# Performance work log

Hardware: AMD Instinct MI355X
Metric: run time of the kernel (lower is better)

The kernel has to match this reference:

```python
import jax, jax.numpy as jnp
import numpy as np

B, S, H, OUT = 4096, 200, 512, 64


def setup_inputs() -> dict:
    key = jax.random.key(0)
    ks = jax.random.split(key, 16)
    sc = 0.05
    return {
        "last_input": jax.random.normal(ks[0], (B, OUT), jnp.float32),
        "hidden": jax.random.normal(ks[1], (1, B, H), jnp.float32),
        "encoder_outputs": jax.random.normal(ks[2], (S, B, H), jnp.float32),
        "attn_W": jax.random.normal(ks[3], (S, H + OUT), jnp.float32) * sc,
        "attn_b": jax.random.normal(ks[4], (S,), jnp.float32) * sc,
        "comb_W": jax.random.normal(ks[5], (H, H + OUT), jnp.float32) * sc,
        "comb_b": jax.random.normal(ks[6], (H,), jnp.float32) * sc,
        "w_ih": jax.random.normal(ks[7], (3 * H, H), jnp.float32) * sc,
        "w_hh": jax.random.normal(ks[8], (3 * H, H), jnp.float32) * sc,
        "b_ih": jax.random.normal(ks[9], (3 * H,), jnp.float32) * sc,
        "b_hh": jax.random.normal(ks[10], (3 * H,), jnp.float32) * sc,
        "out_W": jax.random.normal(ks[11], (OUT, H), jnp.float32) * sc,
        "out_b": jax.random.normal(ks[12], (OUT,), jnp.float32) * sc,
    }


def reference(last_input, hidden, encoder_outputs, attn_W, attn_b, comb_W,
              comb_b, w_ih, w_hh, b_ih, b_hh, out_W, out_b):
    h0 = hidden[0]  # [B,H]
    # Bahdanau-style attention scores over the encoder sequence
    cat1 = jnp.concatenate([last_input, h0], axis=1)          # [B, OUT+H]
    attn_weights = jax.nn.softmax(cat1 @ attn_W.T + attn_b, axis=1)  # [B,S]
    enc = jnp.transpose(encoder_outputs, (1, 0, 2))            # [B,S,H]
    attn_applied = jnp.einsum('bs,bsh->bh', attn_weights, enc)  # [B,H]
    # combine + relu
    cat2 = jnp.concatenate([last_input, attn_applied], axis=1)  # [B, OUT+H]
    x = jax.nn.relu(cat2 @ comb_W.T + comb_b)                   # [B,H]
    # single-step GRU (PyTorch gate order: r, z, n)
    gi = x @ w_ih.T + b_ih                                      # [B,3H]
    gh = h0 @ w_hh.T + b_hh                                     # [B,3H]
    i_r, i_z, i_n = jnp.split(gi, 3, axis=1)
    h_r, h_z, h_n = jnp.split(gh, 3, axis=1)
    r = jax.nn.sigmoid(i_r + h_r)
    z = jax.nn.sigmoid(i_z + h_z)
    n = jnp.tanh(i_n + r * h_n)
    h_new = (1.0 - z) * n + z * h0                              # [B,H]
    out = h_new @ out_W.T + out_b                               # [B,OUT]
    return out, h_new[None], attn_weights
```

## Files before the change

### kernel.cpp

```cpp
#include <hip/hip_runtime.h>
#include <cstddef>

constexpr int Bn = 4096;
constexpr int Sn = 200;
constexpr int Hn = 512;
constexpr int On = 64;
constexpr int K1 = 576;

constexpr size_t HNEW_OFF = (size_t)Bn * On;
constexpr size_t AW_OFF   = (size_t)Bn * On + (size_t)Bn * Hn;

constexpr size_t CAT1B_OFF = 0;
constexpr size_t CAT2B_OFF = CAT1B_OFF + (size_t)Bn * K1 * 2;
constexpr size_t XB_OFF    = CAT2B_OFF + (size_t)Bn * K1 * 2;
constexpr size_t WIHB_OFF  = XB_OFF    + (size_t)Bn * Hn * 2;
constexpr size_t WHHB_OFF  = WIHB_OFF  + (size_t)3 * Hn * Hn * 2;
constexpr size_t CWB_OFF   = WHHB_OFF  + (size_t)3 * Hn * Hn * 2;
constexpr size_t OWB_OFF   = CWB_OFF   + (size_t)Hn * K1 * 2;
constexpr size_t AWB_OFF   = OWB_OFF   + (size_t)On * Hn * 2;
constexpr size_t LOG_OFF   = AWB_OFF   + (size_t)256 * K1 * 2;
constexpr size_t HNB_OFF   = LOG_OFF   + (size_t)Bn * Sn * 4;

typedef __attribute__((ext_vector_type(8))) short bf16x8;
typedef __attribute__((ext_vector_type(4))) float f32x4;

__device__ __forceinline__ float sigmoidf_(float v) { return 1.f / (1.f + __expf(-v)); }
__device__ __forceinline__ unsigned short f2bf(float f) {
    unsigned u = __float_as_uint(f);
    return (unsigned short)((u + 0x7FFFu + ((u >> 16) & 1u)) >> 16);
}
__device__ __forceinline__ ushort4 pack4(float4 v) {
    ushort4 o = { f2bf(v.x), f2bf(v.y), f2bf(v.z), f2bf(v.w) };
    return o;
}

__global__ __launch_bounds__(256) void cvt_all_kernel(
    const float* __restrict__ hidden, const float* __restrict__ wih,
    const float* __restrict__ whh, const float* __restrict__ combW,
    const float* __restrict__ outW, const float* __restrict__ attnW,
    const float* __restrict__ li,
    unsigned short* __restrict__ cat1b, unsigned short* __restrict__ cat2b,
    unsigned short* __restrict__ wihb, unsigned short* __restrict__ whhb,
    unsigned short* __restrict__ combWb, unsigned short* __restrict__ outWb,
    unsigned short* __restrict__ awWb)
{
    const int blk = blockIdx.x;
    const int t = threadIdx.x;
    if (blk < 2048) {
        size_t off = (size_t)blk * 1024 + (size_t)t * 4;
        int b = (int)(off >> 9), col = (int)(off & 511);
        float4 v = *(const float4*)(hidden + off);
        *(ushort4*)(cat1b + (size_t)b * K1 + On + col) = pack4(v);
    } else if (blk < 3584) {
        size_t off = (size_t)(blk - 2048) * 1024 + (size_t)t * 4;
        const float* s = (blk < 2816) ? wih : whh;
        unsigned short* d = (blk < 2816) ? wihb : whhb;
        if (blk >= 2816) off -= (size_t)768 * 1024;
        float4 v = *(const float4*)(s + off);
        *(ushort4*)(d + off) = pack4(v);
    } else if (blk < 3872) {
        size_t off = (size_t)(blk - 3584) * 1024 + (size_t)t * 4;
        float4 v = *(const float4*)(combW + off);
        *(ushort4*)(combWb + off) = pack4(v);
    } else if (blk < 3904) {
        size_t off = (size_t)(blk - 3872) * 1024 + (size_t)t * 4;
        float4 v = *(const float4*)(outW + off);
        *(ushort4*)(outWb + off) = pack4(v);
    } else if (blk < 4017) {
        size_t off = (size_t)(blk - 3904) * 1024 + (size_t)t * 4;
        if (off < (size_t)Sn * K1) {
            float4 v = *(const float4*)(attnW + off);
            *(ushort4*)(awWb + off) = pack4(v);
        }
    } else if (blk < 4049) {
        size_t off = (size_t)Sn * K1 + (size_t)(blk - 4017) * 1024 + (size_t)t * 4;
        if (off < (size_t)256 * K1) {
            ushort4 z = {0, 0, 0, 0};
            *(ushort4*)(awWb + off) = z;
        }
    } else {
        size_t off = (size_t)(blk - 4049) * 1024 + (size_t)t * 4;
        int b = (int)(off >> 6), col = (int)(off & 63);
        float4 v = *(const float4*)(li + off);
        ushort4 o = pack4(v);
        *(ushort4*)(cat1b + (size_t)b * K1 + col) = o;
        *(ushort4*)(cat2b + (size_t)b * K1 + col) = o;
    }
}

template<int MF, int NF, bool RELU, bool OUT_BF16>
__device__ __forceinline__ void gemm_bt_body(
    const unsigned short* __restrict__ A, int lda,
    const unsigned short* __restrict__ B,
    const float* __restrict__ bias, float* __restrict__ Cf,
    unsigned short* __restrict__ Cb, int K, int ldc,
    int m0, int n0, int nmax)
{
    constexpr int BM = 32 * MF;
    constexpr int BN = 32 * NF;
    __shared__ unsigned short As[BM * 64];
    __shared__ unsigned short Bs[BN * 64];

    const int tid = threadIdx.x;
    const int wave = tid >> 6;
    const int lane = tid & 63;
    const int wm = wave >> 1, wn = wave & 1;
    const int l15 = lane & 15, lg = lane >> 4;

    f32x4 acc[MF][NF];
#pragma unroll
    for (int i = 0; i < MF; ++i)
#pragma unroll
        for (int j = 0; j < NF; ++j) acc[i][j] = (f32x4){0.f, 0.f, 0.f, 0.f};

    for (int kc = 0; kc < K; kc += 64) {
        __syncthreads();
#pragma unroll
        for (int i = 0; i < BM * 8 / 256; ++i) {
            int idx = tid + i * 256;
            int row = idx >> 3, ck = idx & 7;
            uint4 v = *(const uint4*)(A + (size_t)(m0 + row) * lda + kc + ck * 8);
            int byte = row * 128 + ((ck * 16) ^ ((row & 7) << 4));
            *(uint4*)((char*)As + byte) = v;
        }
#pragma unroll
        for (int i = 0; i < BN * 8 / 256; ++i) {
            int idx = tid + i * 256;
            int row = idx >> 3, ck = idx & 7;
            uint4 v = *(const uint4*)(B + (size_t)(n0 + row) * K + kc + ck * 8);
            int byte = row * 128 + ((ck * 16) ^ ((row & 7) << 4));
            *(uint4*)((char*)Bs + byte) = v;
        }
        __syncthreads();
#pragma unroll
        for (int s = 0; s < 2; ++s) {
            bf16x8 af[MF], bfr[NF];
#pragma unroll
            for (int i = 0; i < MF; ++i) {
                int row = wm * (MF * 16) + i * 16 + l15;
                int byte = row * 128 + ((s * 64 + lg * 16) ^ ((row & 7) << 4));
                af[i] = *(const bf16x8*)((const char*)As + byte);
            }
#pragma unroll
            for (int j = 0; j < NF; ++j) {
                int row = wn * (NF * 16) + j * 16 + l15;
                int byte = row * 128 + ((s * 64 + lg * 16) ^ ((row & 7) << 4));
                bfr[j] = *(const bf16x8*)((const char*)Bs + byte);
            }
#pragma unroll
            for (int i = 0; i < MF; ++i)
#pragma unroll
                for (int j = 0; j < NF; ++j)
                    acc[i][j] = __builtin_amdgcn_mfma_f32_16x16x32_bf16(
                        af[i], bfr[j], acc[i][j], 0, 0, 0);
        }
    }

#pragma unroll
    for (int i = 0; i < MF; ++i) {
        int m = m0 + wm * (MF * 16) + i * 16 + lg * 4;
#pragma unroll
        for (int j = 0; j < NF; ++j) {
            int n = n0 + wn * (NF * 16) + j * 16 + l15;
            if (n < nmax) {
                float bv = bias[n];
#pragma unroll
                for (int r = 0; r < 4; ++r) {
                    float v = acc[i][j][r] + bv;
                    if (RELU) v = fmaxf(v, 0.f);
                    if (OUT_BF16) Cb[(size_t)(m + r) * ldc + n] = f2bf(v);
                    else          Cf[(size_t)(m + r) * ldc + n] = v;
                }
            }
        }
    }
}

__global__ __launch_bounds__(256, 2) void scores_gemm_kernel(
    const unsigned short* __restrict__ cat1b, const unsigned short* __restrict__ awWb,
    const float* __restrict__ attn_b, float* __restrict__ logits)
{
    gemm_bt_body<2, 2, false, false>(cat1b, K1, awWb, attn_b, logits, nullptr,
                                     K1, Sn, blockIdx.x * 64, blockIdx.y * 64, Sn);
}

__global__ __launch_bounds__(256, 2) void comb_gemm_kernel(
    const unsigned short* __restrict__ cat2b, const unsigned short* __restrict__ combWb,
    const float* __restrict__ comb_b, unsigned short* __restrict__ xb)
{
    gemm_bt_body<4, 4, true, true>(cat2b, K1, combWb, comb_b, nullptr, xb,
                                   K1, Hn, blockIdx.x * 128, blockIdx.y * 128, Hn);
}

__global__ __launch_bounds__(256, 2) void out_gemm_kernel(
    const unsigned short* __restrict__ hnewb, const unsigned short* __restrict__ outWb,
    const float* __restrict__ out_b, float* __restrict__ dout)
{
    gemm_bt_body<4, 2, false, false>(hnewb, Hn, outWb, out_b, dout, nullptr,
                                     Hn, On, blockIdx.x * 128, 0, On);
}

__global__ __launch_bounds__(256) void softmax_kernel(
    const float* __restrict__ logits, float* __restrict__ dout)
{
    const int row = blockIdx.x * 4 + (threadIdx.x >> 6);
    const int lane = threadIdx.x & 63;
    const float* lp = logits + (size_t)row * Sn;
    float v[4], e[4];
    float m = -3.0e38f;
#pragma unroll
    for (int k = 0; k < 4; ++k) {
        int s = lane + 64 * k;
        v[k] = (s < Sn) ? lp[s] : -3.0e38f;
        m = fmaxf(m, v[k]);
    }
#pragma unroll
    for (int o = 32; o > 0; o >>= 1) m = fmaxf(m, __shfl_xor(m, o, 64));
    float sum = 0.f;
#pragma unroll
    for (int k = 0; k < 4; ++k) {
        int s = lane + 64 * k;
        e[k] = (s < Sn) ? __expf(v[k] - m) : 0.f;
        sum += e[k];
    }
#pragma unroll
    for (int o = 32; o > 0; o >>= 1) sum += __shfl_xor(sum, o, 64);
    float inv = 1.f / sum;
#pragma unroll
    for (int k = 0; k < 4; ++k) {
        int s = lane + 64 * k;
        if (s < Sn) dout[AW_OFF + (size_t)row * Sn + s] = e[k] * inv;
    }
}

__global__ __launch_bounds__(256) void attn_apply_kernel(
    const float* __restrict__ enc, const float* __restrict__ aw,
    unsigned short* __restrict__ cat2b)
{
    __shared__ float wl[8 * Sn];
    const int tid = threadIdx.x;
    const int b0 = blockIdx.x * 8;

    for (int idx = tid; idx < 8 * Sn; idx += 256)
        wl[idx] = aw[(size_t)b0 * Sn + idx];
    __syncthreads();

    const int q = tid >> 7;
    const int hc = tid & 127;
    const f32x4* base = (const f32x4*)enc + ((size_t)(b0 + q * 4)) * 128 + hc;

    f32x4 a0 = {0,0,0,0}, a1 = {0,0,0,0}, a2 = {0,0,0,0}, a3 = {0,0,0,0};

#pragma unroll 2
    for (int s = 0; s < Sn; ++s) {
        const f32x4* p = base + (size_t)s * (Bn * 128);
        f32x4 v0 = __builtin_nontemporal_load(p);
        f32x4 v1 = __builtin_nontemporal_load(p + 128);
        f32x4 v2 = __builtin_nontemporal_load(p + 256);
        f32x4 v3 = __builtin_nontemporal_load(p + 384);
        float w0 = wl[(q * 4 + 0) * Sn + s];
        float w1 = wl[(q * 4 + 1) * Sn + s];
        float w2 = wl[(q * 4 + 2) * Sn + s];
        float w3 = wl[(q * 4 + 3) * Sn + s];
        a0 += v0 * w0; a1 += v1 * w1; a2 += v2 * w2; a3 += v3 * w3;
    }

    const int h = hc * 4;
    f32x4 accs[4] = {a0, a1, a2, a3};
#pragma unroll
    for (int r = 0; r < 4; ++r) {
        ushort4 o = { f2bf(accs[r][0]), f2bf(accs[r][1]), f2bf(accs[r][2]), f2bf(accs[r][3]) };
        *(ushort4*)(cat2b + (size_t)(b0 + q * 4 + r) * K1 + On + h) = o;
    }
}

__device__ __forceinline__ void gru_gemm_phase(
    const unsigned short* __restrict__ A, int lda,
    const unsigned short* __restrict__ W,
    int m0, int n0, int tid, int wm, int wn, int l15, int lg,
    unsigned short* As, unsigned short* Bs,
    f32x4 aR[2][2], f32x4 aZ[2][2], f32x4 aN[2][2])
{
    for (int kc = 0; kc < Hn; kc += 64) {
        __syncthreads();
#pragma unroll
        for (int i = 0; i < 2; ++i) {
            int idx = tid + i * 256;
            int row = idx >> 3, ck = idx & 7;
            uint4 v = *(const uint4*)(A + (size_t)(m0 + row) * lda + kc + ck * 8);
            int byte = row * 128 + ((ck * 16) ^ ((row & 7) << 4));
            *(uint4*)((char*)As + byte) = v;
        }
#pragma unroll
        for (int g = 0; g < 3; ++g)
#pragma unroll
            for (int i = 0; i < 2; ++i) {
                int idx = tid + i * 256;
                int row = idx >> 3, ck = idx & 7;
                uint4 v = *(const uint4*)(W + (size_t)(g * Hn + n0 + row) * Hn + kc + ck * 8);
                int byte = row * 128 + ((ck * 16) ^ ((row & 7) << 4));
                *(uint4*)((char*)Bs + g * 8192 + byte) = v;
            }
        __syncthreads();
#pragma unroll
        for (int s = 0; s < 2; ++s) {
            bf16x8 af[2], bf0[2], bf1[2], bf2[2];
#pragma unroll
            for (int i = 0; i < 2; ++i) {
                int row = wm * 32 + i * 16 + l15;
                int byte = row * 128 + ((s * 64 + lg * 16) ^ ((row & 7) << 4));
                af[i] = *(const bf16x8*)((const char*)As + byte);
            }
#pragma unroll
            for (int j = 0; j < 2; ++j) {
                int row = wn * 32 + j * 16 + l15;
                int byte = row * 128 + ((s * 64 + lg * 16) ^ ((row & 7) << 4));
                bf0[j] = *(const bf16x8*)((const char*)Bs + 0 * 8192 + byte);
                bf1[j] = *(const bf16x8*)((const char*)Bs + 1 * 8192 + byte);
                bf2[j] = *(const bf16x8*)((const char*)Bs + 2 * 8192 + byte);
            }
#pragma unroll
            for (int i = 0; i < 2; ++i)
#pragma unroll
                for (int j = 0; j < 2; ++j) {
                    aR[i][j] = __builtin_amdgcn_mfma_f32_16x16x32_bf16(af[i], bf0[j], aR[i][j], 0, 0, 0);
                    aZ[i][j] = __builtin_amdgcn_mfma_f32_16x16x32_bf16(af[i], bf1[j], aZ[i][j], 0, 0, 0);
                    aN[i][j] = __builtin_amdgcn_mfma_f32_16x16x32_bf16(af[i], bf2[j], aN[i][j], 0, 0, 0);
                }
        }
    }
}

__global__ __launch_bounds__(256, 2) void gru_fused_kernel(
    const unsigned short* __restrict__ xb, const unsigned short* __restrict__ cat1b,
    const unsigned short* __restrict__ wihb, const unsigned short* __restrict__ whhb,
    const float* __restrict__ b_ih, const float* __restrict__ b_hh,
    const float* __restrict__ hidden,
    float* __restrict__ dout, unsigned short* __restrict__ hnewb)
{
    __shared__ unsigned short As[64 * 64];
    __shared__ unsigned short Bs[3 * 64 * 64];

    const int tid = threadIdx.x;
    const int m0 = blockIdx.x * 64;
    const int n0 = blockIdx.y * 64;
    const int wave = tid >> 6, lane = tid & 63;
    const int wm = wave >> 1, wn = wave & 1;
    const int l15 = lane & 15, lg = lane >> 4;

    f32x4 aR[2][2], aZ[2][2], aN0[2][2], aN1[2][2];
#pragma unroll
    for (int i = 0; i < 2; ++i)
#pragma unroll
        for (int j = 0; j < 2; ++j) {
            aR[i][j] = (f32x4){0.f, 0.f, 0.f, 0.f};
            aZ[i][j] = (f32x4){0.f, 0.f, 0.f, 0.f};
            aN0[i][j] = (f32x4){0.f, 0.f, 0.f, 0.f};
            aN1[i][j] = (f32x4){0.f, 0.f, 0.f, 0.f};
        }

    gru_gemm_phase(xb, Hn, wihb, m0, n0, tid, wm, wn, l15, lg, As, Bs, aR, aZ, aN0);
    gru_gemm_phase(cat1b + On, K1, whhb, m0, n0, tid, wm, wn, l15, lg, As, Bs, aR, aZ, aN1);

#pragma unroll
    for (int j = 0; j < 2; ++j) {
        const int n = n0 + wn * 32 + j * 16 + l15;
        const float bR = b_ih[n] + b_hh[n];
        const float bZ = b_ih[Hn + n] + b_hh[Hn + n];
        const float bI = b_ih[2 * Hn + n];
        const float bH = b_hh[2 * Hn + n];
#pragma unroll
        for (int i = 0; i < 2; ++i) {
            const int mb = m0 + wm * 32 + i * 16 + lg * 4;
#pragma unroll
            for (int r = 0; r < 4; ++r) {
                const int m = mb + r;
                float h0 = hidden[(size_t)m * Hn + n];
                float rg = sigmoidf_(aR[i][j][r] + bR);
                float zg = sigmoidf_(aZ[i][j][r] + bZ);
                float ng = tanhf(aN0[i][j][r] + bI + rg * (aN1[i][j][r] + bH));
                float o = (1.f - zg) * ng + zg * h0;
                dout[HNEW_OFF + (size_t)m * Hn + n] = o;
                hnewb[(size_t)m * Hn + n] = f2bf(o);
            }
        }
    }
}

extern "C" void kernel_launch(void* const* d_in, const int* in_sizes, int n_in,
                              void* d_out, int out_size, void* d_ws, size_t ws_size,
                              hipStream_t stream)
{
    const float* last_input = (const float*)d_in[0];
    const float* hidden     = (const float*)d_in[1];
    const float* enc        = (const float*)d_in[2];
    const float* attn_W     = (const float*)d_in[3];
    const float* attn_b     = (const float*)d_in[4];
    const float* comb_W     = (const float*)d_in[5];
    const float* comb_b     = (const float*)d_in[6];
    const float* w_ih       = (const float*)d_in[7];
    const float* w_hh       = (const float*)d_in[8];
    const float* b_ih       = (const float*)d_in[9];
    const float* b_hh       = (const float*)d_in[10];
    const float* out_W      = (const float*)d_in[11];
    const float* out_b      = (const float*)d_in[12];

    float* out = (float*)d_out;
    char*  ws  = (char*)d_ws;
    unsigned short* cat1b  = (unsigned short*)(ws + CAT1B_OFF);
    unsigned short* cat2b  = (unsigned short*)(ws + CAT2B_OFF);
    unsigned short* xb     = (unsigned short*)(ws + XB_OFF);
    unsigned short* wihb   = (unsigned short*)(ws + WIHB_OFF);
    unsigned short* whhb   = (unsigned short*)(ws + WHHB_OFF);
    unsigned short* combWb = (unsigned short*)(ws + CWB_OFF);
    unsigned short* outWb  = (unsigned short*)(ws + OWB_OFF);
    unsigned short* awWb   = (unsigned short*)(ws + AWB_OFF);
    float*          logits = (float*)(ws + LOG_OFF);
    unsigned short* hnewb  = (unsigned short*)(ws + HNB_OFF);

    cvt_all_kernel<<<4305, 256, 0, stream>>>(hidden, w_ih, w_hh, comb_W, out_W,
                                             attn_W, last_input,
                                             cat1b, cat2b, wihb, whhb, combWb,
                                             outWb, awWb);
    scores_gemm_kernel<<<dim3(Bn / 64, 4), 256, 0, stream>>>(cat1b, awWb, attn_b, logits);
    softmax_kernel<<<Bn / 4, 256, 0, stream>>>(logits, out);
    attn_apply_kernel<<<Bn / 8, 256, 0, stream>>>(enc, out + AW_OFF, cat2b);
    comb_gemm_kernel<<<dim3(Bn / 128, Hn / 128), 256, 0, stream>>>(cat2b, combWb, comb_b, xb);
    gru_fused_kernel<<<dim3(Bn / 64, Hn / 64), 256, 0, stream>>>(
        xb, cat1b, wihb, whhb, b_ih, b_hh, hidden, out, hnewb);
    out_gemm_kernel<<<Bn / 128, 256, 0, stream>>>(hnewb, outWb, out_b, out);
}
```

Baseline: 323.4 us.

## Hoist GRU hidden-side GEMM into scores kernel and overlap weight conversion

The h0·W_hh GEMM no longer runs inside the GRU kernel. It is computed early, in the same launch as the attention-score GEMM, and stored as a bf16 gh buffer. That launch also converts the w_ih, comb_W and out_W weights, which removes that conversion from the first kernel's critical path. The GRU kernel now does only the x·W_ih GEMM plus the gate math, reading gh from memory. The trade-offs are extra global traffic for the gh buffer, rounding of gh to bf16 which changes numerics slightly, and relu/out_bf16 becoming runtime flags instead of template parameters.

```diff
diff --git a/kernel.cpp b/kernel.cpp
--- a/kernel.cpp
+++ b/kernel.cpp
@@ -19,7 +19,8 @@
 constexpr size_t OWB_OFF   = CWB_OFF   + (size_t)Hn * K1 * 2;
 constexpr size_t AWB_OFF   = OWB_OFF   + (size_t)On * Hn * 2;
 constexpr size_t LOG_OFF   = AWB_OFF   + (size_t)256 * K1 * 2;
-constexpr size_t HNB_OFF   = LOG_OFF   + (size_t)Bn * Sn * 4;
+constexpr size_t GHB_OFF   = LOG_OFF   + (size_t)Bn * Sn * 4;
+constexpr size_t HNB_OFF   = GHB_OFF   + (size_t)Bn * 3 * Hn * 2;
 
 typedef __attribute__((ext_vector_type(8))) short bf16x8;
 typedef __attribute__((ext_vector_type(4))) float f32x4;
@@ -29,20 +30,19 @@
     unsigned u = __float_as_uint(f);
     return (unsigned short)((u + 0x7FFFu + ((u >> 16) & 1u)) >> 16);
 }
+__device__ __forceinline__ float bf2f(unsigned short b) {
+    return __uint_as_float((unsigned)b << 16);
+}
 __device__ __forceinline__ ushort4 pack4(float4 v) {
     ushort4 o = { f2bf(v.x), f2bf(v.y), f2bf(v.z), f2bf(v.w) };
     return o;
 }
 
-__global__ __launch_bounds__(256) void cvt_all_kernel(
-    const float* __restrict__ hidden, const float* __restrict__ wih,
-    const float* __restrict__ whh, const float* __restrict__ combW,
-    const float* __restrict__ outW, const float* __restrict__ attnW,
-    const float* __restrict__ li,
+__global__ __launch_bounds__(256) void cvt_min_kernel(
+    const float* __restrict__ hidden, const float* __restrict__ whh,
+    const float* __restrict__ attnW, const float* __restrict__ li,
     unsigned short* __restrict__ cat1b, unsigned short* __restrict__ cat2b,
-    unsigned short* __restrict__ wihb, unsigned short* __restrict__ whhb,
-    unsigned short* __restrict__ combWb, unsigned short* __restrict__ outWb,
-    unsigned short* __restrict__ awWb)
+    unsigned short* __restrict__ whhb, unsigned short* __restrict__ awWb)
 {
     const int blk = blockIdx.x;
     const int t = threadIdx.x;
@@ -51,35 +51,24 @@
         int b = (int)(off >> 9), col = (int)(off & 511);
         float4 v = *(const float4*)(hidden + off);
         *(ushort4*)(cat1b + (size_t)b * K1 + On + col) = pack4(v);
-    } else if (blk < 3584) {
+    } else if (blk < 2816) {
         size_t off = (size_t)(blk - 2048) * 1024 + (size_t)t * 4;
-        const float* s = (blk < 2816) ? wih : whh;
-        unsigned short* d = (blk < 2816) ? wihb : whhb;
-        if (blk >= 2816) off -= (size_t)768 * 1024;
-        float4 v = *(const float4*)(s + off);
-        *(ushort4*)(d + off) = pack4(v);
-    } else if (blk < 3872) {
-        size_t off = (size_t)(blk - 3584) * 1024 + (size_t)t * 4;
-        float4 v = *(const float4*)(combW + off);
-        *(ushort4*)(combWb + off) = pack4(v);
-    } else if (blk < 3904) {
-        size_t off = (size_t)(blk - 3872) * 1024 + (size_t)t * 4;
-        float4 v = *(const float4*)(outW + off);
-        *(ushort4*)(outWb + off) = pack4(v);
-    } else if (blk < 4017) {
-        size_t off = (size_t)(blk - 3904) * 1024 + (size_t)t * 4;
+        float4 v = *(const float4*)(whh + off);
+        *(ushort4*)(whhb + off) = pack4(v);
+    } else if (blk < 2929) {
+        size_t off = (size_t)(blk - 2816) * 1024 + (size_t)t * 4;
         if (off < (size_t)Sn * K1) {
             float4 v = *(const float4*)(attnW + off);
             *(ushort4*)(awWb + off) = pack4(v);
         }
-    } else if (blk < 4049) {
-        size_t off = (size_t)Sn * K1 + (size_t)(blk - 4017) * 1024 + (size_t)t * 4;
+    } else if (blk < 2961) {
+        size_t off = (size_t)Sn * K1 + (size_t)(blk - 2929) * 1024 + (size_t)t * 4;
         if (off < (size_t)256 * K1) {
             ushort4 z = {0, 0, 0, 0};
             *(ushort4*)(awWb + off) = z;
         }
     } else {
-        size_t off = (size_t)(blk - 4049) * 1024 + (size_t)t * 4;
+        size_t off = (size_t)(blk - 2961) * 1024 + (size_t)t * 4;
         int b = (int)(off >> 6), col = (int)(off & 63);
         float4 v = *(const float4*)(li + off);
         ushort4 o = pack4(v);
@@ -88,13 +77,13 @@
     }
 }
 
-template<int MF, int NF, bool RELU, bool OUT_BF16>
+template<int MF, int NF>
 __device__ __forceinline__ void gemm_bt_body(
     const unsigned short* __restrict__ A, int lda,
     const unsigned short* __restrict__ B,
     const float* __restrict__ bias, float* __restrict__ Cf,
     unsigned short* __restrict__ Cb, int K, int ldc,
-    int m0, int n0, int nmax)
+    int m0, int n0, int nmax, bool relu, bool out_bf16)
 {
     constexpr int BM = 32 * MF;
     constexpr int BN = 32 * NF;
@@ -167,8 +156,8 @@
 #pragma unroll
                 for (int r = 0; r < 4; ++r) {
                     float v = acc[i][j][r] + bv;
-                    if (RELU) v = fmaxf(v, 0.f);
-                    if (OUT_BF16) Cb[(size_t)(m + r) * ldc + n] = f2bf(v);
+                    if (relu) v = fmaxf(v, 0.f);
+                    if (out_bf16) Cb[(size_t)(m + r) * ldc + n] = f2bf(v);
                     else          Cf[(size_t)(m + r) * ldc + n] = v;
                 }
             }
@@ -176,28 +165,65 @@
     }
 }
 
-__global__ __launch_bounds__(256, 2) void scores_gemm_kernel(
+__global__ __launch_bounds__(256, 2) void scores_gh_cvt_kernel(
     const unsigned short* __restrict__ cat1b, const unsigned short* __restrict__ awWb,
-    const float* __restrict__ attn_b, float* __restrict__ logits)
-{
-    gemm_bt_body<2, 2, false, false>(cat1b, K1, awWb, attn_b, logits, nullptr,
-                                     K1, Sn, blockIdx.x * 64, blockIdx.y * 64, Sn);
+    const float* __restrict__ attn_b, float* __restrict__ logits,
+    const unsigned short* __restrict__ whhb, const float* __restrict__ b_hh,
+    unsigned short* __restrict__ ghb,
+    const float* __restrict__ wih, const float* __restrict__ combW,
+    const float* __restrict__ outW,
+    unsigned short* __restrict__ wihb, unsigned short* __restrict__ combWb,
+    unsigned short* __restrict__ outWb)
+{
+    const int blk = blockIdx.x;
+    if (blk < 448) {
+        const bool is_gh = (blk >= 64);
+        const int qq = is_gh ? (blk - 64) : blk;
+        const int m0 = (qq & 31) * 128;
+        const int n0 = (qq >> 5) * 128;
+        gemm_bt_body<4, 4>(
+            is_gh ? (cat1b + On) : cat1b, K1,
+            is_gh ? whhb : awWb,
+            is_gh ? b_hh : attn_b,
+            logits, ghb,
+            is_gh ? Hn : K1,
+            is_gh ? 3 * Hn : Sn,
+            m0, n0,
+            is_gh ? 3 * Hn : Sn,
+            false, is_gh);
+    } else {
+        const int r = blk - 448;
+        const int t = threadIdx.x;
+        if (r < 768) {
+            size_t off = (size_t)r * 1024 + (size_t)t * 4;
+            float4 v = *(const float4*)(wih + off);
+            *(ushort4*)(wihb + off) = pack4(v);
+        } else if (r < 1056) {
+            size_t off = (size_t)(r - 768) * 1024 + (size_t)t * 4;
+            float4 v = *(const float4*)(combW + off);
+            *(ushort4*)(combWb + off) = pack4(v);
+        } else {
+            size_t off = (size_t)(r - 1056) * 1024 + (size_t)t * 4;
+            float4 v = *(const float4*)(outW + off);
+            *(ushort4*)(outWb + off) = pack4(v);
+        }
+    }
 }
 
 __global__ __launch_bounds__(256, 2) void comb_gemm_kernel(
     const unsigned short* __restrict__ cat2b, const unsigned short* __restrict__ combWb,
     const float* __restrict__ comb_b, unsigned short* __restrict__ xb)
 {
-    gemm_bt_body<4, 4, true, true>(cat2b, K1, combWb, comb_b, nullptr, xb,
-                                   K1, Hn, blockIdx.x * 128, blockIdx.y * 128, Hn);
+    gemm_bt_body<4, 4>(cat2b, K1, combWb, comb_b, nullptr, xb,
+                       K1, Hn, blockIdx.x * 128, blockIdx.y * 128, Hn, true, true);
 }
 
 __global__ __launch_bounds__(256, 2) void out_gemm_kernel(
     const unsigned short* __restrict__ hnewb, const unsigned short* __restrict__ outWb,
     const float* __restrict__ out_b, float* __restrict__ dout)
 {
-    gemm_bt_body<4, 2, false, false>(hnewb, Hn, outWb, out_b, dout, nullptr,
-                                     Hn, On, blockIdx.x * 128, 0, On);
+    gemm_bt_body<4, 2>(hnewb, Hn, outWb, out_b, dout, nullptr,
+                       Hn, On, blockIdx.x * 128, 0, On, false, false);
 }
 
 __global__ __launch_bounds__(256) void softmax_kernel(
@@ -331,10 +357,9 @@
     }
 }
 
-__global__ __launch_bounds__(256, 2) void gru_fused_kernel(
-    const unsigned short* __restrict__ xb, const unsigned short* __restrict__ cat1b,
-    const unsigned short* __restrict__ wihb, const unsigned short* __restrict__ whhb,
-    const float* __restrict__ b_ih, const float* __restrict__ b_hh,
+__global__ __launch_bounds__(256, 2) void gru_gi_kernel(
+    const unsigned short* __restrict__ xb, const unsigned short* __restrict__ wihb,
+    const float* __restrict__ b_ih, const unsigned short* __restrict__ ghb,
     const float* __restrict__ hidden,
     float* __restrict__ dout, unsigned short* __restrict__ hnewb)
 {
@@ -348,37 +373,38 @@
     const int wm = wave >> 1, wn = wave & 1;
     const int l15 = lane & 15, lg = lane >> 4;
 
-    f32x4 aR[2][2], aZ[2][2], aN0[2][2], aN1[2][2];
+    f32x4 aR[2][2], aZ[2][2], aN[2][2];
 #pragma unroll
     for (int i = 0; i < 2; ++i)
 #pragma unroll
         for (int j = 0; j < 2; ++j) {
             aR[i][j] = (f32x4){0.f, 0.f, 0.f, 0.f};
             aZ[i][j] = (f32x4){0.f, 0.f, 0.f, 0.f};
-            aN0[i][j] = (f32x4){0.f, 0.f, 0.f, 0.f};
-            aN1[i][j] = (f32x4){0.f, 0.f, 0.f, 0.f};
-        }
-
-    gru_gemm_phase(xb, Hn, wihb, m0, n0, tid, wm, wn, l15, lg, As, Bs, aR, aZ, aN0);
-    gru_gemm_phase(cat1b + On, K1, whhb, m0, n0, tid, wm, wn, l15, lg, As, Bs, aR, aZ, aN1);
+            aN[i][j] = (f32x4){0.f, 0.f, 0.f, 0.f};
+        }
+
+    gru_gemm_phase(xb, Hn, wihb, m0, n0, tid, wm, wn, l15, lg, As, Bs, aR, aZ, aN);
 
 #pragma unroll
     for (int j = 0; j < 2; ++j) {
         const int n = n0 + wn * 32 + j * 16 + l15;
-        const float bR = b_ih[n] + b_hh[n];
-        const float bZ = b_ih[Hn + n] + b_hh[Hn + n];
+        const float bR = b_ih[n];
+        const float bZ = b_ih[Hn + n];
         const float bI = b_ih[2 * Hn + n];
-        const float bH = b_hh[2 * Hn + n];
 #pragma unroll
         for (int i = 0; i < 2; ++i) {
             const int mb = m0 + wm * 32 + i * 16 + lg * 4;
 #pragma unroll
             for (int r = 0; r < 4; ++r) {
                 const int m = mb + r;
-                float h0 = hidden[(size_t)m * Hn + n];
-                float rg = sigmoidf_(aR[i][j][r] + bR);
-                float zg = sigmoidf_(aZ[i][j][r] + bZ);
-                float ng = tanhf(aN0[i][j][r] + bI + rg * (aN1[i][j][r] + bH));
+                const unsigned short* gh = ghb + (size_t)m * (3 * Hn);
+                float h0  = hidden[(size_t)m * Hn + n];
+                float ghr = bf2f(gh[n]);
+                float ghz = bf2f(gh[Hn + n]);
+                float ghn = bf2f(gh[2 * Hn + n]);
+                float rg = sigmoidf_(aR[i][j][r] + bR + ghr);
+                float zg = sigmoidf_(aZ[i][j][r] + bZ + ghz);
+                float ng = tanhf(aN[i][j][r] + bI + rg * ghn);
                 float o = (1.f - zg) * ng + zg * h0;
                 dout[HNEW_OFF + (size_t)m * Hn + n] = o;
                 hnewb[(size_t)m * Hn + n] = f2bf(o);
@@ -416,17 +442,19 @@
     unsigned short* outWb  = (unsigned short*)(ws + OWB_OFF);
     unsigned short* awWb   = (unsigned short*)(ws + AWB_OFF);
     float*          logits = (float*)(ws + LOG_OFF);
+    unsigned short* ghb    = (unsigned short*)(ws + GHB_OFF);
     unsigned short* hnewb  = (unsigned short*)(ws + HNB_OFF);
 
-    cvt_all_kernel<<<4305, 256, 0, stream>>>(hidden, w_ih, w_hh, comb_W, out_W,
-                                             attn_W, last_input,
-                                             cat1b, cat2b, wihb, whhb, combWb,
-                                             outWb, awWb);
-    scores_gemm_kernel<<<dim3(Bn / 64, 4), 256, 0, stream>>>(cat1b, awWb, attn_b, logits);
+    cvt_min_kernel<<<3217, 256, 0, stream>>>(hidden, w_hh, attn_W, last_input,
+                                             cat1b, cat2b, whhb, awWb);
+    scores_gh_cvt_kernel<<<1536, 256, 0, stream>>>(cat1b, awWb, attn_b, logits,
+                                                   whhb, b_hh, ghb,
+                                                   w_ih, comb_W, out_W,
+                                                   wihb, combWb, outWb);
     softmax_kernel<<<Bn / 4, 256, 0, stream>>>(logits, out);
     attn_apply_kernel<<<Bn / 8, 256, 0, stream>>>(enc, out + AW_OFF, cat2b);
     comb_gemm_kernel<<<dim3(Bn / 128, Hn / 128), 256, 0, stream>>>(cat2b, combWb, comb_b, xb);
-    gru_fused_kernel<<<dim3(Bn / 64, Hn / 64), 256, 0, stream>>>(
-        xb, cat1b, wihb, whhb, b_ih, b_hh, hidden, out, hnewb);
+    gru_gi_kernel<<<dim3(Bn / 64, Hn / 64), 256, 0, stream>>>(
+        xb, wihb, b_ih, ghb, hidden, out, hnewb);
     out_gemm_kernel<<<Bn / 128, 256, 0, stream>>>(hnewb, outWb, out_b, out);
 }
```

New measurement: 329.9 us. 1.02x slower.
